# Performance work log

Hardware: AMD Instinct MI355X
Metric: run time of the kernel (lower is better)

Reference implementation:

```python
import jax, jax.numpy as jnp
import numpy as np

U, I, D, L = 100000, 100000, 64, 50
B, T = 4096, 100


def setup_inputs() -> dict:
    key = jax.random.key(0)
    ks = jax.random.split(key, 12)
    inp = {}
    inp["item_seq"] = jax.random.randint(ks[0], (B, L), 0, I, dtype=jnp.int64 if jax.config.jax_enable_x64 else jnp.int32)
    inp["user_ids"] = jax.random.randint(ks[1], (B,), 0, U, dtype=jnp.int32)
    inp["items_to_predict"] = jax.random.randint(ks[2], (B, T), 0, I, dtype=jnp.int32)
    # parameters (match torch inits: N(0, 1/d) embeddings, xavier gates, zero b2)
    inp["user_emb_table"] = jax.random.normal(ks[3], (U, D), jnp.float32) / D
    inp["item_emb_table"] = jax.random.normal(ks[4], (I, D), jnp.float32) / D
    lin_s = float(np.sqrt(1.0 / D))
    inp["fg_item_W"] = jax.random.uniform(ks[5], (D, D), jnp.float32, -lin_s, lin_s)
    inp["fg_item_b"] = jax.random.uniform(ks[6], (D,), jnp.float32, -lin_s, lin_s)
    inp["fg_user_W"] = jax.random.uniform(ks[7], (D, D), jnp.float32, -lin_s, lin_s)
    inp["fg_user_b"] = jax.random.uniform(ks[8], (D,), jnp.float32, -lin_s, lin_s)
    xg1 = float(np.sqrt(6.0 / (D + 1)))
    xg2 = float(np.sqrt(6.0 / (D + L)))
    inp["instance_gate_item"] = jax.random.uniform(ks[9], (D, 1), jnp.float32, -xg1, xg1)
    inp["instance_gate_user"] = jax.random.uniform(ks[10], (D, L), jnp.float32, -xg2, xg2)
    W2 = jax.random.normal(ks[11], (I, D), jnp.float32) / D
    inp["W2_table"] = W2.at[0].set(0.0)  # padding_idx=0
    inp["b2_table"] = jnp.zeros((I, 1), jnp.float32)
    return inp


def reference(item_seq, user_ids, items_to_predict, user_emb_table, item_emb_table,
              fg_item_W, fg_item_b, fg_user_W, fg_user_b,
              instance_gate_item, instance_gate_user, W2_table, b2_table):
    item_embs = item_emb_table[item_seq]          # [B, L, D]
    user_emb = user_emb_table[user_ids]           # [B, D]
    # feature gating
    gate = jax.nn.sigmoid(item_embs @ fg_item_W + fg_item_b
                          + (user_emb @ fg_user_W + fg_user_b)[:, None, :])
    gated_item = item_embs * gate                 # [B, L, D]
    # instance gating
    instance_score = jax.nn.sigmoid(
        jnp.einsum('bld,d->bl', gated_item, instance_gate_item[:, 0])
        + user_emb @ instance_gate_user)          # [B, L]
    union_out = jnp.sum(gated_item * instance_score[..., None], axis=1)
    union_out = union_out / jnp.sum(instance_score, axis=1, keepdims=True)  # [B, D]
    # scoring (for_pred=False branch)
    w2 = W2_table[items_to_predict]               # [B, T, D]
    b2 = b2_table[items_to_predict][..., 0]       # [B, T]
    res = b2 + jnp.einsum('btd,bd->bt', w2, user_emb)
    res = res + jnp.einsum('btd,bd->bt', w2, union_out)
    # rel_score: sum_l item_embs @ w2^T == (sum_l item_embs) . w2
    res = res + jnp.einsum('bd,btd->bt', item_embs.sum(axis=1), w2)
    return res
```

## Files before the change

kernel.cpp:

```cpp
#include <hip/hip_runtime.h>

#define D_ 64
#define L_ 50
#define B_ 4096
#define T_ 100
#define SP 65
#define RS 72

typedef __attribute__((ext_vector_type(8))) short  short8;
typedef __attribute__((ext_vector_type(4))) float  float4v;
typedef __attribute__((ext_vector_type(4))) unsigned short ushort4v;

__device__ __forceinline__ float sigmoidf_(float x) {
    return 1.0f / (1.0f + __expf(-x));
}
__device__ __forceinline__ unsigned short f2bf(float x) {
    unsigned u = __builtin_bit_cast(unsigned, x);
    return (unsigned short)((u + 0x7fffu + ((u >> 16) & 1u)) >> 16);
}
__device__ __forceinline__ float bf2f(unsigned short s) {
    return __builtin_bit_cast(float, (unsigned)s << 16);
}

__global__ __launch_bounds__(256) void hgn_transpose_w(
    const float* __restrict__ fg_item_W, unsigned short* __restrict__ wbT)
{
    const int i = blockIdx.x * 256 + threadIdx.x;
    const int k = i >> 6, c = i & 63;
    wbT[c * 64 + k] = f2bf(fg_item_W[i]);
}

__global__ __launch_bounds__(256) void hgn_fused_kernel(
    const int* __restrict__ item_seq,
    const int* __restrict__ user_ids,
    const int* __restrict__ items_to_predict,
    const float* __restrict__ user_emb_table,
    const float* __restrict__ item_emb_table,
    const unsigned short* __restrict__ wbT,
    const float* __restrict__ fg_item_b,
    const float* __restrict__ fg_user_W,
    const float* __restrict__ fg_user_b,
    const float* __restrict__ ig_item,
    const float* __restrict__ ig_user,
    const float* __restrict__ W2,
    const float* __restrict__ b2,
    float* __restrict__ out)
{
    __shared__ unsigned short eb_sh[64 * RS];
    __shared__ float part_sh[L_ * SP];
    __shared__ __align__(16) float u_sh[D_];
    __shared__ __align__(16) float v_sh[D_];
    __shared__ float gb_sh[D_];
    __shared__ float s_sh[L_];
    __shared__ float bp_sh[2][64];
    __shared__ float esum_sh[D_];
    __shared__ int   idx_sh[L_];

    const int t    = threadIdx.x;
    const int lane = t & 63;
    const int wave = t >> 6;
    const int b    = blockIdx.x;

    if (t < L_) idx_sh[t] = item_seq[b * L_ + t];
    if (t >= 64 && t < 128) {
        const int uid = user_ids[b];
        u_sh[t - 64] = user_emb_table[(size_t)uid * D_ + (t - 64)];
    }
    __syncthreads();

    if (wave == 3) {
        float g0 = fg_item_b[lane], g1 = fg_user_b[lane], g2 = 0.f, g3 = 0.f;
#pragma unroll
        for (int k = 0; k < D_; k += 4) {
            g0 = fmaf(u_sh[k + 0], fg_user_W[(k + 0) * D_ + lane], g0);
            g1 = fmaf(u_sh[k + 1], fg_user_W[(k + 1) * D_ + lane], g1);
            g2 = fmaf(u_sh[k + 2], fg_user_W[(k + 2) * D_ + lane], g2);
            g3 = fmaf(u_sh[k + 3], fg_user_W[(k + 3) * D_ + lane], g3);
        }
        gb_sh[lane] = (g0 + g1) + (g2 + g3);
    } else {
        for (int i = t; i < L_ * 16; i += 192) {
            const int l = i >> 4, qd = i & 15;
            const float4 r = ((const float4*)(item_emb_table + (size_t)idx_sh[l] * D_))[qd];
            ushort4v o = { f2bf(r.x), f2bf(r.y), f2bf(r.z), f2bf(r.w) };
            *(ushort4v*)&eb_sh[l * RS + qd * 4] = o;
        }
    }
    __syncthreads();

    {
        const int m = lane & 15, q = lane >> 4;
        const int arow = 16 * wave + m;
        const short8 a0 = *(const short8*)&eb_sh[arow * RS + q * 8];
        const short8 a1 = *(const short8*)&eb_sh[arow * RS + 32 + q * 8];
#pragma unroll
        for (int n = 0; n < 4; ++n) {
            const int col = 16 * n + m;
            const short8 b0 = *(const short8*)&wbT[col * 64 + q * 8];
            const short8 b1 = *(const short8*)&wbT[col * 64 + 32 + q * 8];
            float4v acc = {0.f, 0.f, 0.f, 0.f};
            acc = __builtin_amdgcn_mfma_f32_16x16x32_bf16(a0, b0, acc, 0, 0, 0);
            acc = __builtin_amdgcn_mfma_f32_16x16x32_bf16(a1, b1, acc, 0, 0, 0);
            const float gbc = gb_sh[col];
#pragma unroll
            for (int r = 0; r < 4; ++r) {
                const int l = 16 * wave + q * 4 + r;
                if (l < L_) {
                    const float e = bf2f(eb_sh[l * RS + col]);
                    part_sh[l * SP + col] = e * sigmoidf_(acc[r] + gbc);
                }
            }
        }
    }
    __syncthreads();

    if (wave < 2) {
        if (lane < L_) {
            const int d0 = 32 * wave;
            float p0 = 0.f, p1 = 0.f, p2 = 0.f, p3 = 0.f;
#pragma unroll
            for (int j = 0; j < 32; j += 4) {
                const int d = d0 + j;
                p0 = fmaf(part_sh[lane * SP + d + 0], ig_item[d + 0], p0);
                p1 = fmaf(part_sh[lane * SP + d + 1], ig_item[d + 1], p1);
                p2 = fmaf(part_sh[lane * SP + d + 2], ig_item[d + 2], p2);
                p3 = fmaf(part_sh[lane * SP + d + 3], ig_item[d + 3], p3);
                p0 = fmaf(u_sh[d + 0], ig_user[(d + 0) * L_ + lane], p0);
                p1 = fmaf(u_sh[d + 1], ig_user[(d + 1) * L_ + lane], p1);
                p2 = fmaf(u_sh[d + 2], ig_user[(d + 2) * L_ + lane], p2);
                p3 = fmaf(u_sh[d + 3], ig_user[(d + 3) * L_ + lane], p3);
            }
            bp_sh[wave][lane] = (p0 + p1) + (p2 + p3);
        }
    } else if (wave == 2) {
        float e0 = 0.f, e1 = 0.f;
#pragma unroll
        for (int l = 0; l < L_; l += 2) {
            e0 += bf2f(eb_sh[l * RS + lane]);
            e1 += bf2f(eb_sh[(l + 1) * RS + lane]);
        }
        esum_sh[lane] = e0 + e1;
    }
    __syncthreads();

    if (wave == 0) {
        if (lane < L_) s_sh[lane] = sigmoidf_(bp_sh[0][lane] + bp_sh[1][lane]);
        float a0 = 0.f, a1 = 0.f, ss = 0.f;
        for (int l = 0; l < L_; l += 2) {
            const float sA = s_sh[l], sB = s_sh[l + 1];
            a0 = fmaf(part_sh[l * SP + lane], sA, a0);
            a1 = fmaf(part_sh[(l + 1) * SP + lane], sB, a1);
            ss += sA + sB;
        }
        v_sh[lane] = u_sh[lane] + (a0 + a1) / ss + esum_sh[lane];
    }
    __syncthreads();

    if (t < 2 * T_) {
        const int tt = t >> 1, half = t & 1;
        const int idx = items_to_predict[b * T_ + tt];
        const float* wrow  = W2 + (size_t)idx * D_ + half * 32;
        const float* vhalf = v_sh + half * 32;
        float r0 = 0.f, r1 = 0.f, r2 = 0.f, r3 = 0.f;
#pragma unroll
        for (int kk = 0; kk < 8; ++kk) {
            const float4 w4 = ((const float4*)wrow)[kk];
            const float4 v4 = ((const float4*)vhalf)[kk];
            r0 = fmaf(v4.x, w4.x, r0);
            r1 = fmaf(v4.y, w4.y, r1);
            r2 = fmaf(v4.z, w4.z, r2);
            r3 = fmaf(v4.w, w4.w, r3);
        }
        float r = (r0 + r1) + (r2 + r3);
        r += __shfl_xor(r, 1, 64);
        if (half == 0) out[b * T_ + tt] = r + b2[idx];
    }
}

extern "C" void kernel_launch(void* const* d_in, const int* in_sizes, int n_in,
                              void* d_out, int out_size, void* d_ws, size_t ws_size,
                              hipStream_t stream) {
    const int*   item_seq   = (const int*)d_in[0];
    const int*   user_ids   = (const int*)d_in[1];
    const int*   items_pred = (const int*)d_in[2];
    const float* uet        = (const float*)d_in[3];
    const float* iet        = (const float*)d_in[4];
    const float* fgiW       = (const float*)d_in[5];
    const float* fgib       = (const float*)d_in[6];
    const float* fguW       = (const float*)d_in[7];
    const float* fgub       = (const float*)d_in[8];
    const float* igi        = (const float*)d_in[9];
    const float* igu        = (const float*)d_in[10];
    const float* W2         = (const float*)d_in[11];
    const float* b2t        = (const float*)d_in[12];

    unsigned short* wbT = (unsigned short*)d_ws;

    hgn_transpose_w<<<16, 256, 0, stream>>>(fgiW, wbT);
    hgn_fused_kernel<<<B_, 256, 0, stream>>>(
        item_seq, user_ids, items_pred, uet, iet,
        wbT, fgib, fguW, fgub, igi, igu, W2, b2t, (float*)d_out);
}
```

Baseline: 165.3 us.

## Pre-convert embedding and W2 tables to bf16 and prefetch W2 rows early

Adds a pass that converts the full item embedding table and W2 table to bf16 in workspace each call, so the main kernel gathers half-width rows. The W2 rows and b2 are loaded into registers at kernel start to overlap their latency with the gating computation. A fallback keeps the old kernel when the workspace is too small. The full-table conversion adds streaming traffic per call that may offset the cheaper gathers, and W2 precision drops to bf16.

```diff
diff --git a/kernel.cpp b/kernel.cpp
--- a/kernel.cpp
+++ b/kernel.cpp
@@ -22,6 +22,17 @@
     return __builtin_bit_cast(float, (unsigned)s << 16);
 }
 
+__global__ __launch_bounds__(256) void hgn_cvt_bf16(
+    const float4* __restrict__ src, ushort4v* __restrict__ dst, int n4)
+{
+    const int i = blockIdx.x * 256 + threadIdx.x;
+    if (i < n4) {
+        const float4 r = src[i];
+        ushort4v o = { f2bf(r.x), f2bf(r.y), f2bf(r.z), f2bf(r.w) };
+        dst[i] = o;
+    }
+}
+
 __global__ __launch_bounds__(256) void hgn_transpose_w(
     const float* __restrict__ fg_item_W, unsigned short* __restrict__ wbT)
 {
@@ -30,19 +41,19 @@
     wbT[c * 64 + k] = f2bf(fg_item_W[i]);
 }
 
-__global__ __launch_bounds__(256) void hgn_fused_kernel(
+__global__ __launch_bounds__(256) void hgn_fused_main(
     const int* __restrict__ item_seq,
     const int* __restrict__ user_ids,
     const int* __restrict__ items_to_predict,
     const float* __restrict__ user_emb_table,
-    const float* __restrict__ item_emb_table,
+    const unsigned short* __restrict__ ebf,
     const unsigned short* __restrict__ wbT,
     const float* __restrict__ fg_item_b,
     const float* __restrict__ fg_user_W,
     const float* __restrict__ fg_user_b,
     const float* __restrict__ ig_item,
     const float* __restrict__ ig_user,
-    const float* __restrict__ W2,
+    const unsigned short* __restrict__ w2bf,
     const float* __restrict__ b2,
     float* __restrict__ out)
 {
@@ -54,21 +65,28 @@
     __shared__ float s_sh[L_];
     __shared__ float bp_sh[2][64];
     __shared__ float esum_sh[D_];
-    __shared__ int   idx_sh[L_];
 
     const int t    = threadIdx.x;
     const int lane = t & 63;
     const int wave = t >> 6;
     const int b    = blockIdx.x;
 
-    if (t < L_) idx_sh[t] = item_seq[b * L_ + t];
-    if (t >= 64 && t < 128) {
+    short8 w2r0, w2r1, w2r2, w2r3;
+    float b2v = 0.f;
+    const int tt = t >> 1, half = t & 1;
+    if (t < 2 * T_) {
+        const int idxp = items_to_predict[b * T_ + tt];
+        const unsigned short* wr = w2bf + (size_t)idxp * D_ + half * 32;
+        w2r0 = *(const short8*)(wr + 0);
+        w2r1 = *(const short8*)(wr + 8);
+        w2r2 = *(const short8*)(wr + 16);
+        w2r3 = *(const short8*)(wr + 24);
+        b2v  = b2[idxp];
+    }
+
+    if (wave == 3) {
         const int uid = user_ids[b];
-        u_sh[t - 64] = user_emb_table[(size_t)uid * D_ + (t - 64)];
-    }
-    __syncthreads();
-
-    if (wave == 3) {
+        u_sh[lane] = user_emb_table[(size_t)uid * D_ + lane];
         float g0 = fg_item_b[lane], g1 = fg_user_b[lane], g2 = 0.f, g3 = 0.f;
 #pragma unroll
         for (int k = 0; k < D_; k += 4) {
@@ -79,12 +97,17 @@
         }
         gb_sh[lane] = (g0 + g1) + (g2 + g3);
     } else {
-        for (int i = t; i < L_ * 16; i += 192) {
-            const int l = i >> 4, qd = i & 15;
-            const float4 r = ((const float4*)(item_emb_table + (size_t)idx_sh[l] * D_))[qd];
-            ushort4v o = { f2bf(r.x), f2bf(r.y), f2bf(r.z), f2bf(r.w) };
-            *(ushort4v*)&eb_sh[l * RS + qd * 4] = o;
-        }
+        const int i0 = t, i1 = t + 192, i2 = t + 384;
+        const int id0 = item_seq[b * L_ + (i0 >> 3)];
+        const int id1 = item_seq[b * L_ + (i1 >> 3)];
+        const int id2 = (i2 < 400) ? item_seq[b * L_ + (i2 >> 3)] : 0;
+        const short8 r0 = *(const short8*)(ebf + (size_t)id0 * D_ + (i0 & 7) * 8);
+        const short8 r1 = *(const short8*)(ebf + (size_t)id1 * D_ + (i1 & 7) * 8);
+        short8 r2;
+        if (i2 < 400) r2 = *(const short8*)(ebf + (size_t)id2 * D_ + (i2 & 7) * 8);
+        *(short8*)&eb_sh[(i0 >> 3) * RS + (i0 & 7) * 8] = r0;
+        *(short8*)&eb_sh[(i1 >> 3) * RS + (i1 & 7) * 8] = r1;
+        if (i2 < 400) *(short8*)&eb_sh[(i2 >> 3) * RS + (i2 & 7) * 8] = r2;
     }
     __syncthreads();
 
@@ -156,6 +179,134 @@
     }
     __syncthreads();
 
+    if (t < 2 * T_) {
+        const float* vh = v_sh + half * 32;
+        float a0 = 0.f, a1 = 0.f, a2 = 0.f, a3 = 0.f;
+#pragma unroll
+        for (int j = 0; j < 8; ++j) {
+            a0 = fmaf(bf2f((unsigned short)w2r0[j]), vh[j + 0],  a0);
+            a1 = fmaf(bf2f((unsigned short)w2r1[j]), vh[j + 8],  a1);
+            a2 = fmaf(bf2f((unsigned short)w2r2[j]), vh[j + 16], a2);
+            a3 = fmaf(bf2f((unsigned short)w2r3[j]), vh[j + 24], a3);
+        }
+        float r = (a0 + a1) + (a2 + a3);
+        r += __shfl_xor(r, 1, 64);
+        if (half == 0) out[b * T_ + tt] = r + b2v;
+    }
+}
+
+__global__ __launch_bounds__(256) void hgn_fused_fallback(
+    const int* __restrict__ item_seq, const int* __restrict__ user_ids,
+    const int* __restrict__ items_to_predict,
+    const float* __restrict__ user_emb_table, const float* __restrict__ item_emb_table,
+    const unsigned short* __restrict__ wbT, const float* __restrict__ fg_item_b,
+    const float* __restrict__ fg_user_W, const float* __restrict__ fg_user_b,
+    const float* __restrict__ ig_item, const float* __restrict__ ig_user,
+    const float* __restrict__ W2, const float* __restrict__ b2,
+    float* __restrict__ out)
+{
+    __shared__ unsigned short eb_sh[64 * RS];
+    __shared__ float part_sh[L_ * SP];
+    __shared__ __align__(16) float u_sh[D_];
+    __shared__ __align__(16) float v_sh[D_];
+    __shared__ float gb_sh[D_];
+    __shared__ float s_sh[L_];
+    __shared__ float bp_sh[2][64];
+    __shared__ float esum_sh[D_];
+    __shared__ int   idx_sh[L_];
+
+    const int t = threadIdx.x, lane = t & 63, wave = t >> 6, b = blockIdx.x;
+
+    if (t < L_) idx_sh[t] = item_seq[b * L_ + t];
+    if (t >= 64 && t < 128) {
+        const int uid = user_ids[b];
+        u_sh[t - 64] = user_emb_table[(size_t)uid * D_ + (t - 64)];
+    }
+    __syncthreads();
+    if (wave == 3) {
+        float g0 = fg_item_b[lane], g1 = fg_user_b[lane], g2 = 0.f, g3 = 0.f;
+#pragma unroll
+        for (int k = 0; k < D_; k += 4) {
+            g0 = fmaf(u_sh[k + 0], fg_user_W[(k + 0) * D_ + lane], g0);
+            g1 = fmaf(u_sh[k + 1], fg_user_W[(k + 1) * D_ + lane], g1);
+            g2 = fmaf(u_sh[k + 2], fg_user_W[(k + 2) * D_ + lane], g2);
+            g3 = fmaf(u_sh[k + 3], fg_user_W[(k + 3) * D_ + lane], g3);
+        }
+        gb_sh[lane] = (g0 + g1) + (g2 + g3);
+    } else {
+        for (int i = t; i < L_ * 16; i += 192) {
+            const int l = i >> 4, qd = i & 15;
+            const float4 r = ((const float4*)(item_emb_table + (size_t)idx_sh[l] * D_))[qd];
+            ushort4v o = { f2bf(r.x), f2bf(r.y), f2bf(r.z), f2bf(r.w) };
+            *(ushort4v*)&eb_sh[l * RS + qd * 4] = o;
+        }
+    }
+    __syncthreads();
+    {
+        const int m = lane & 15, q = lane >> 4;
+        const int arow = 16 * wave + m;
+        const short8 a0 = *(const short8*)&eb_sh[arow * RS + q * 8];
+        const short8 a1 = *(const short8*)&eb_sh[arow * RS + 32 + q * 8];
+#pragma unroll
+        for (int n = 0; n < 4; ++n) {
+            const int col = 16 * n + m;
+            const short8 b0 = *(const short8*)&wbT[col * 64 + q * 8];
+            const short8 b1 = *(const short8*)&wbT[col * 64 + 32 + q * 8];
+            float4v acc = {0.f, 0.f, 0.f, 0.f};
+            acc = __builtin_amdgcn_mfma_f32_16x16x32_bf16(a0, b0, acc, 0, 0, 0);
+            acc = __builtin_amdgcn_mfma_f32_16x16x32_bf16(a1, b1, acc, 0, 0, 0);
+            const float gbc = gb_sh[col];
+#pragma unroll
+            for (int r = 0; r < 4; ++r) {
+                const int l = 16 * wave + q * 4 + r;
+                if (l < L_) {
+                    const float e = bf2f(eb_sh[l * RS + col]);
+                    part_sh[l * SP + col] = e * sigmoidf_(acc[r] + gbc);
+                }
+            }
+        }
+    }
+    __syncthreads();
+    if (wave < 2) {
+        if (lane < L_) {
+            const int d0 = 32 * wave;
+            float p0 = 0.f, p1 = 0.f, p2 = 0.f, p3 = 0.f;
+#pragma unroll
+            for (int j = 0; j < 32; j += 4) {
+                const int d = d0 + j;
+                p0 = fmaf(part_sh[lane * SP + d + 0], ig_item[d + 0], p0);
+                p1 = fmaf(part_sh[lane * SP + d + 1], ig_item[d + 1], p1);
+                p2 = fmaf(part_sh[lane * SP + d + 2], ig_item[d + 2], p2);
+                p3 = fmaf(part_sh[lane * SP + d + 3], ig_item[d + 3], p3);
+                p0 = fmaf(u_sh[d + 0], ig_user[(d + 0) * L_ + lane], p0);
+                p1 = fmaf(u_sh[d + 1], ig_user[(d + 1) * L_ + lane], p1);
+                p2 = fmaf(u_sh[d + 2], ig_user[(d + 2) * L_ + lane], p2);
+                p3 = fmaf(u_sh[d + 3], ig_user[(d + 3) * L_ + lane], p3);
+            }
+            bp_sh[wave][lane] = (p0 + p1) + (p2 + p3);
+        }
+    } else if (wave == 2) {
+        float e0 = 0.f, e1 = 0.f;
+#pragma unroll
+        for (int l = 0; l < L_; l += 2) {
+            e0 += bf2f(eb_sh[l * RS + lane]);
+            e1 += bf2f(eb_sh[(l + 1) * RS + lane]);
+        }
+        esum_sh[lane] = e0 + e1;
+    }
+    __syncthreads();
+    if (wave == 0) {
+        if (lane < L_) s_sh[lane] = sigmoidf_(bp_sh[0][lane] + bp_sh[1][lane]);
+        float a0 = 0.f, a1 = 0.f, ss = 0.f;
+        for (int l = 0; l < L_; l += 2) {
+            const float sA = s_sh[l], sB = s_sh[l + 1];
+            a0 = fmaf(part_sh[l * SP + lane], sA, a0);
+            a1 = fmaf(part_sh[(l + 1) * SP + lane], sB, a1);
+            ss += sA + sB;
+        }
+        v_sh[lane] = u_sh[lane] + (a0 + a1) / ss + esum_sh[lane];
+    }
+    __syncthreads();
     if (t < 2 * T_) {
         const int tt = t >> 1, half = t & 1;
         const int idx = items_to_predict[b * T_ + tt];
@@ -194,10 +345,28 @@
     const float* W2         = (const float*)d_in[11];
     const float* b2t        = (const float*)d_in[12];
 
-    unsigned short* wbT = (unsigned short*)d_ws;
-
-    hgn_transpose_w<<<16, 256, 0, stream>>>(fgiW, wbT);
-    hgn_fused_kernel<<<B_, 256, 0, stream>>>(
-        item_seq, user_ids, items_pred, uet, iet,
-        wbT, fgib, fguW, fgub, igi, igu, W2, b2t, (float*)d_out);
-}
+    const size_t tbl_elems = 100000 * 64;
+    const size_t tbl_bytes = tbl_elems * 2;
+    const size_t need = 2 * tbl_bytes + 8192;
+
+    if (ws_size >= need) {
+        unsigned short* w2bf = (unsigned short*)d_ws;
+        unsigned short* ebf  = (unsigned short*)((char*)d_ws + tbl_bytes);
+        unsigned short* wbT  = (unsigned short*)((char*)d_ws + 2 * tbl_bytes);
+        const int n4 = (int)(tbl_elems / 4);
+        hgn_cvt_bf16<<<(n4 + 255) / 256, 256, 0, stream>>>(
+            (const float4*)W2,  (ushort4v*)w2bf, n4);
+        hgn_cvt_bf16<<<(n4 + 255) / 256, 256, 0, stream>>>(
+            (const float4*)iet, (ushort4v*)ebf,  n4);
+        hgn_transpose_w<<<16, 256, 0, stream>>>(fgiW, wbT);
+        hgn_fused_main<<<B_, 256, 0, stream>>>(
+            item_seq, user_ids, items_pred, uet, ebf, wbT,
+            fgib, fguW, fgub, igi, igu, w2bf, b2t, (float*)d_out);
+    } else {
+        unsigned short* wbT = (unsigned short*)d_ws;
+        hgn_transpose_w<<<16, 256, 0, stream>>>(fgiW, wbT);
+        hgn_fused_fallback<<<B_, 256, 0, stream>>>(
+            item_seq, user_ids, items_pred, uet, iet,
+            wbT, fgib, fguW, fgub, igi, igu, W2, b2t, (float*)d_out);
+    }
+}
```

Result: no change. 166.6 us (+0.7%).
